# Kernel optimization log

Hardware: AMD Instinct MI355X
Metric: run time of the kernel (lower is better)

Reference implementation:

```python
import jax, jax.numpy as jnp
import numpy as np

N_NODES = 100000
N_EDGES = 640000
D_IN = 128
D_OUT = 128


def setup_inputs() -> dict:
    key = jax.random.key(0)
    k1, k2, k3, k4, k5 = jax.random.split(key, 5)
    feats = jax.random.normal(k1, (N_NODES, D_IN), dtype=jnp.float32)
    src = jax.random.randint(k2, (N_EDGES,), 0, N_NODES, dtype=jnp.int32)
    dst = jax.random.randint(k3, (N_EDGES,), 0, N_NODES, dtype=jnp.int32)
    # Xavier-normal-ish init (gain for relu = sqrt(2))
    std = float(np.sqrt(2.0) * np.sqrt(2.0 / (D_IN + D_OUT)))
    linear_skip_weight = jax.random.normal(k4, (D_OUT, D_IN), dtype=jnp.float32) * std
    linear_msg_weight = jax.random.normal(k5, (D_OUT, D_IN), dtype=jnp.float32) * std
    linear_skip_bias = jnp.zeros((D_OUT,), dtype=jnp.float32)
    linear_msg_bias = jnp.zeros((D_OUT,), dtype=jnp.float32)
    return {
        "feats": feats,
        "src": src,
        "dst": dst,
        "linear_skip_weight": linear_skip_weight,
        "linear_skip_bias": linear_skip_bias,
        "linear_msg_weight": linear_msg_weight,
        "linear_msg_bias": linear_msg_bias,
    }


def reference(feats, src, dst, linear_skip_weight, linear_skip_bias,
              linear_msg_weight, linear_msg_bias):
    n = feats.shape[0]
    # degree from scatter-add of edge weights (ones) at source rows
    deg = jax.ops.segment_sum(jnp.ones_like(src, dtype=feats.dtype), src,
                              num_segments=n)
    deg_inv_sqrt = jnp.where(deg > 0, jax.lax.rsqrt(jnp.maximum(deg, 1.0)) * (deg > 0), 0.0)
    deg_inv_sqrt = jnp.where(deg > 0, deg ** -0.5, 0.0)
    # normalize source features, gather along edges, scatter-sum to dst
    feat_src = feats * deg_inv_sqrt[:, None]           # [N, D_IN]
    msgs = feat_src[src]                               # [E, D_IN]
    rst = jax.ops.segment_sum(msgs, dst, num_segments=n)  # [N, D_IN]
    rst = rst * deg_inv_sqrt[:, None]
    rst_ = rst @ linear_msg_weight.T + linear_msg_bias
    skip_x = feats @ linear_skip_weight.T + linear_skip_bias
    return rst_ + skip_x
```

## Files before the change

### kernel.cpp

```cpp
#include <hip/hip_runtime.h>

#define N_NODES 100000
#define N_EDGES 640000
#define D 128
#define NB ((N_NODES + 1023) / 1024)
#define BKT_C 16
#define OVF_CAP 32768

typedef short v8s __attribute__((ext_vector_type(8)));
typedef float v4f __attribute__((ext_vector_type(4)));

__device__ __forceinline__ unsigned short f2bf(float x) {
    unsigned int u = __builtin_bit_cast(unsigned int, x);
    u += 0x7fffu + ((u >> 16) & 1u);
    return (unsigned short)(u >> 16);
}
__device__ __forceinline__ float bf2f(unsigned int hi) {
    return __builtin_bit_cast(float, hi << 16);
}

__global__ __launch_bounds__(256) void k_zero(int4* __restrict__ pk4,
                                              int* __restrict__ ovf_cnt) {
    int i = blockIdx.x * blockDim.x + threadIdx.x;
    if (i < N_NODES / 4) pk4[i] = make_int4(0, 0, 0, 0);
    if (i == 0) *ovf_cnt = 0;
}

__global__ __launch_bounds__(256) void k_pre(const float* __restrict__ feats,
                                             const float* __restrict__ Wm,
                                             const float* __restrict__ Ws,
                                             const float* __restrict__ bmsg,
                                             const float* __restrict__ bskip,
                                             const int* __restrict__ src,
                                             const int* __restrict__ dst,
                                             unsigned int* __restrict__ pk,
                                             unsigned short* __restrict__ Bcat,
                                             float* __restrict__ bias,
                                             char* __restrict__ fsbase,
                                             int fs_stride,
                                             int* __restrict__ bucket,
                                             int* __restrict__ ovf_cnt,
                                             int2* __restrict__ ovf) {
    int i = blockIdx.x * blockDim.x + threadIdx.x;
    if (i < D * D) {
        int j = i >> 7;
        int k = i & 127;
        Bcat[j * 256 + k]       = f2bf(Wm[i]);
        Bcat[j * 256 + 128 + k] = f2bf(Ws[i]);
    }
    if (i < D) bias[i] = bmsg[i] + bskip[i];
    if (i < N_EDGES) {
        int s = src[i];
        int d = dst[i];
        atomicAdd(&pk[s], 1u);
        unsigned int old = atomicAdd(&pk[d], 0x10000u);
        if (bucket) {
            unsigned int p = old >> 16;
            if (p < BKT_C) {
                bucket[d * BKT_C + (int)p] = s;
            } else {
                int q = atomicAdd(ovf_cnt, 1);
                if (q < OVF_CAP) ovf[q] = make_int2(d, s);
            }
        }
    }
    int g = i * 8;
    int row = g >> 7;
    int col = g & 127;
    if (row < N_NODES) {
        const float4* sp = (const float4*)(feats + g);
        float4 x = sp[0], y = sp[1];
        uint4 p;
        p.x = (unsigned)f2bf(x.x) | ((unsigned)f2bf(x.y) << 16);
        p.y = (unsigned)f2bf(x.z) | ((unsigned)f2bf(x.w) << 16);
        p.z = (unsigned)f2bf(y.x) | ((unsigned)f2bf(y.y) << 16);
        p.w = (unsigned)f2bf(y.z) | ((unsigned)f2bf(y.w) << 16);
        *(uint4*)(fsbase + (size_t)row * fs_stride + col * 2) = p;
    }
}

__global__ __launch_bounds__(256) void k_fused2(const char* __restrict__ featsh,
                                                const unsigned int* __restrict__ pk,
                                                const int* __restrict__ bucket,
                                                const int* __restrict__ ovf_cnt,
                                                const int2* __restrict__ ovf,
                                                const unsigned short* __restrict__ Bcat,
                                                const float* __restrict__ bias,
                                                float* __restrict__ outf) {
    __shared__ unsigned short aggh[128][132];
    int tid = threadIdx.x;
    int lane = tid & 63;
    int w = tid >> 6;
    int n0 = blockIdx.x * 128;
    int grp = lane >> 4;
    int sub = lane & 15;

#pragma unroll 2
    for (int j = 0; j < 32; ++j) {
        int wid = n0 + w * 32 + j;
        int widc = wid < N_NODES ? wid : N_NODES - 1;
        unsigned int pkn = pk[widc];
        int cnt = (int)(pkn >> 16);
        int m = cnt < BKT_C ? cnt : BKT_C;
        const int* bk = bucket + widc * BKT_C;

        int4 bq = *(const int4*)(bk + grp * 4);
        int e0 = grp * 4;
        bool a0 = e0 < m, a1 = e0 + 1 < m, a2 = e0 + 2 < m, a3 = e0 + 3 < m;
        int sA = a0 ? bq.x : 0; float gA = a0 ? 1.0f : 0.0f;
        int sB = a1 ? bq.y : 0; float gB = a1 ? 1.0f : 0.0f;
        int sC = a2 ? bq.z : 0; float gC = a2 ? 1.0f : 0.0f;
        int sD = a3 ? bq.w : 0; float gD = a3 ? 1.0f : 0.0f;

        unsigned int pA = pk[sA];
        unsigned int pB = pk[sB];
        unsigned int pC = pk[sC];
        unsigned int pD = pk[sD];
        uint4 vA = *(const uint4*)(featsh + (size_t)sA * 256 + sub * 16);
        uint4 vB = *(const uint4*)(featsh + (size_t)sB * 256 + sub * 16);
        uint4 vC = *(const uint4*)(featsh + (size_t)sC * 256 + sub * 16);
        uint4 vD = *(const uint4*)(featsh + (size_t)sD * 256 + sub * 16);

        float scA = gA * rsqrtf(fmaxf((float)(pA & 0xffffu), 1.0f));
        float scB = gB * rsqrtf(fmaxf((float)(pB & 0xffffu), 1.0f));
        float scC = gC * rsqrtf(fmaxf((float)(pC & 0xffffu), 1.0f));
        float scD = gD * rsqrtf(fmaxf((float)(pD & 0xffffu), 1.0f));

        float acc[8];
#pragma unroll
        for (int i = 0; i < 8; i++) acc[i] = 0.f;
        acc[0] += bf2f(vA.x & 0xffffu) * scA; acc[1] += bf2f(vA.x >> 16) * scA;
        acc[2] += bf2f(vA.y & 0xffffu) * scA; acc[3] += bf2f(vA.y >> 16) * scA;
        acc[4] += bf2f(vA.z & 0xffffu) * scA; acc[5] += bf2f(vA.z >> 16) * scA;
        acc[6] += bf2f(vA.w & 0xffffu) * scA; acc[7] += bf2f(vA.w >> 16) * scA;
        acc[0] += bf2f(vB.x & 0xffffu) * scB; acc[1] += bf2f(vB.x >> 16) * scB;
        acc[2] += bf2f(vB.y & 0xffffu) * scB; acc[3] += bf2f(vB.y >> 16) * scB;
        acc[4] += bf2f(vB.z & 0xffffu) * scB; acc[5] += bf2f(vB.z >> 16) * scB;
        acc[6] += bf2f(vB.w & 0xffffu) * scB; acc[7] += bf2f(vB.w >> 16) * scB;
        acc[0] += bf2f(vC.x & 0xffffu) * scC; acc[1] += bf2f(vC.x >> 16) * scC;
        acc[2] += bf2f(vC.y & 0xffffu) * scC; acc[3] += bf2f(vC.y >> 16) * scC;
        acc[4] += bf2f(vC.z & 0xffffu) * scC; acc[5] += bf2f(vC.z >> 16) * scC;
        acc[6] += bf2f(vC.w & 0xffffu) * scC; acc[7] += bf2f(vC.w >> 16) * scC;
        acc[0] += bf2f(vD.x & 0xffffu) * scD; acc[1] += bf2f(vD.x >> 16) * scD;
        acc[2] += bf2f(vD.y & 0xffffu) * scD; acc[3] += bf2f(vD.y >> 16) * scD;
        acc[4] += bf2f(vD.z & 0xffffu) * scD; acc[5] += bf2f(vD.z >> 16) * scD;
        acc[6] += bf2f(vD.w & 0xffffu) * scD; acc[7] += bf2f(vD.w >> 16) * scD;

        if (cnt > BKT_C) {
            int no = *ovf_cnt;
            if (no > OVF_CAP) no = OVF_CAP;
            for (int i = grp; i < no; i += 4) {
                int2 p = ovf[i];
                if (p.x == widc) {
                    float sc = rsqrtf((float)(pk[p.y] & 0xffffu));
                    uint4 v = *(const uint4*)(featsh + (size_t)p.y * 256 + sub * 16);
                    acc[0] += bf2f(v.x & 0xffffu) * sc; acc[1] += bf2f(v.x >> 16) * sc;
                    acc[2] += bf2f(v.y & 0xffffu) * sc; acc[3] += bf2f(v.y >> 16) * sc;
                    acc[4] += bf2f(v.z & 0xffffu) * sc; acc[5] += bf2f(v.z >> 16) * sc;
                    acc[6] += bf2f(v.w & 0xffffu) * sc; acc[7] += bf2f(v.w >> 16) * sc;
                }
            }
        }

#pragma unroll
        for (int i = 0; i < 8; i++) {
            acc[i] += __shfl_xor(acc[i], 16);
            acc[i] += __shfl_xor(acc[i], 32);
        }
        if (grp == 0) {
            int dsrc = (int)(pkn & 0xffffu);
            float scn = (dsrc > 0) ? rsqrtf((float)dsrc) : 0.0f;
            uint4 p;
            p.x = (unsigned)f2bf(acc[0] * scn) | ((unsigned)f2bf(acc[1] * scn) << 16);
            p.y = (unsigned)f2bf(acc[2] * scn) | ((unsigned)f2bf(acc[3] * scn) << 16);
            p.z = (unsigned)f2bf(acc[4] * scn) | ((unsigned)f2bf(acc[5] * scn) << 16);
            p.w = (unsigned)f2bf(acc[6] * scn) | ((unsigned)f2bf(acc[7] * scn) << 16);
            *(uint4*)(&aggh[w * 32 + j][sub * 8]) = p;
        }
    }

    int q = grp;
    int lr = sub;
    int r0 = n0 + w * 32 + lr;      int r0c = r0 < N_NODES ? r0 : N_NODES - 1;
    int r1 = r0 + 16;               int r1c = r1 < N_NODES ? r1 : N_NODES - 1;
    const char* a0p = featsh + (size_t)r0c * 256 + q * 16;
    const char* a1p = featsh + (size_t)r1c * 256 + q * 16;

    v4f acc2[2][8];
#pragma unroll
    for (int mt = 0; mt < 2; mt++)
#pragma unroll
        for (int t = 0; t < 8; t++) acc2[mt][t] = (v4f){0.f, 0.f, 0.f, 0.f};

#pragma unroll
    for (int kk = 0; kk < 8; kk++) {
        v8s a0, a1;
        if (kk < 4) {
            a0 = *(const v8s*)(&aggh[w * 32 + lr][q * 8 + kk * 32]);
            a1 = *(const v8s*)(&aggh[w * 32 + 16 + lr][q * 8 + kk * 32]);
        } else {
            a0 = *(const v8s*)(a0p + (kk - 4) * 64);
            a1 = *(const v8s*)(a1p + (kk - 4) * 64);
        }
#pragma unroll
        for (int t = 0; t < 8; t++) {
            v8s b = *(const v8s*)(Bcat + (t * 16 + lr) * 256 + kk * 32 + q * 8);
            acc2[0][t] = __builtin_amdgcn_mfma_f32_16x16x32_bf16(a0, b, acc2[0][t], 0, 0, 0);
            acc2[1][t] = __builtin_amdgcn_mfma_f32_16x16x32_bf16(a1, b, acc2[1][t], 0, 0, 0);
        }
    }

#pragma unroll
    for (int t = 0; t < 8; t++) {
        float bv = bias[t * 16 + lr];
#pragma unroll
        for (int mt = 0; mt < 2; mt++) {
            int rowb = n0 + w * 32 + mt * 16 + q * 4;
#pragma unroll
            for (int r = 0; r < 4; r++) {
                int row = rowb + r;
                if (row < N_NODES)
                    outf[(size_t)row * 128 + t * 16 + lr] = acc2[mt][t][r] + bv;
            }
        }
    }
}

__device__ __forceinline__ void agg_edge(const char* outb,
                                         const unsigned int* pk,
                                         int s, int sub, float* acc) {
    float sc = rsqrtf((float)(pk[s] & 0xffffu));
    uint4 v = *(const uint4*)(outb + (size_t)s * 512 + 256 + sub * 16);
    acc[0] += bf2f(v.x & 0xffffu) * sc;
    acc[1] += bf2f(v.x >> 16) * sc;
    acc[2] += bf2f(v.y & 0xffffu) * sc;
    acc[3] += bf2f(v.y >> 16) * sc;
    acc[4] += bf2f(v.z & 0xffffu) * sc;
    acc[5] += bf2f(v.z >> 16) * sc;
    acc[6] += bf2f(v.w & 0xffffu) * sc;
    acc[7] += bf2f(v.w >> 16) * sc;
}

__device__ __forceinline__ void agg_acc(uint4 v, float sc, float* acc) {
    acc[0] += bf2f(v.x & 0xffffu) * sc;
    acc[1] += bf2f(v.x >> 16) * sc;
    acc[2] += bf2f(v.y & 0xffffu) * sc;
    acc[3] += bf2f(v.y >> 16) * sc;
    acc[4] += bf2f(v.z & 0xffffu) * sc;
    acc[5] += bf2f(v.z >> 16) * sc;
    acc[6] += bf2f(v.w & 0xffffu) * sc;
    acc[7] += bf2f(v.w >> 16) * sc;
}

__device__ __forceinline__ void agg_finish(char* outb, int wid,
                                           unsigned int pkn, int grp, int sub,
                                           float* acc) {
#pragma unroll
    for (int i = 0; i < 8; i++) {
        acc[i] += __shfl_xor(acc[i], 16);
        acc[i] += __shfl_xor(acc[i], 32);
    }
    if (grp == 0) {
        int dsrc = (int)(pkn & 0xffffu);
        float scn = (dsrc > 0) ? rsqrtf((float)dsrc) : 0.0f;
        uint4 p;
        p.x = (unsigned)f2bf(acc[0] * scn) | ((unsigned)f2bf(acc[1] * scn) << 16);
        p.y = (unsigned)f2bf(acc[2] * scn) | ((unsigned)f2bf(acc[3] * scn) << 16);
        p.z = (unsigned)f2bf(acc[4] * scn) | ((unsigned)f2bf(acc[5] * scn) << 16);
        p.w = (unsigned)f2bf(acc[6] * scn) | ((unsigned)f2bf(acc[7] * scn) << 16);
        *(uint4*)(outb + (size_t)wid * 512 + sub * 16) = p;
    }
}

__global__ __launch_bounds__(256) void k_agg_bkt(char* __restrict__ outb,
                                                 const unsigned int* __restrict__ pk,
                                                 const int* __restrict__ bucket,
                                                 const int* __restrict__ ovf_cnt,
                                                 const int2* __restrict__ ovf) {
    int wid = (int)((blockIdx.x * (unsigned)blockDim.x + threadIdx.x) >> 6);
    int lane = threadIdx.x & 63;
    if (wid >= N_NODES) return;
    int grp = lane >> 4;
    int sub = lane & 15;
    unsigned int pkn = pk[wid];
    int cnt = (int)(pkn >> 16);
    int m = cnt < BKT_C ? cnt : BKT_C;
    const int* bk = bucket + wid * BKT_C;

    int4 bq = *(const int4*)(bk + grp * 4);
    int e0 = grp * 4;

    bool a0 = e0 < m, a1 = e0 + 1 < m, a2 = e0 + 2 < m, a3 = e0 + 3 < m;
    int sA = a0 ? bq.x : 0; float gA = a0 ? 1.0f : 0.0f;
    int sB = a1 ? bq.y : 0; float gB = a1 ? 1.0f : 0.0f;
    int sC = a2 ? bq.z : 0; float gC = a2 ? 1.0f : 0.0f;
    int sD = a3 ? bq.w : 0; float gD = a3 ? 1.0f : 0.0f;

    unsigned int pA = pk[sA];
    unsigned int pB = pk[sB];
    unsigned int pC = pk[sC];
    unsigned int pD = pk[sD];
    uint4 vA = *(const uint4*)(outb + (size_t)sA * 512 + 256 + sub * 16);
    uint4 vB = *(const uint4*)(outb + (size_t)sB * 512 + 256 + sub * 16);
    uint4 vC = *(const uint4*)(outb + (size_t)sC * 512 + 256 + sub * 16);
    uint4 vD = *(const uint4*)(outb + (size_t)sD * 512 + 256 + sub * 16);

    float scA = gA * rsqrtf(fmaxf((float)(pA & 0xffffu), 1.0f));
    float scB = gB * rsqrtf(fmaxf((float)(pB & 0xffffu), 1.0f));
    float scC = gC * rsqrtf(fmaxf((float)(pC & 0xffffu), 1.0f));
    float scD = gD * rsqrtf(fmaxf((float)(pD & 0xffffu), 1.0f));

    float acc[8];
#pragma unroll
    for (int i = 0; i < 8; i++) acc[i] = 0.f;
    agg_acc(vA, scA, acc);
    agg_acc(vB, scB, acc);
    agg_acc(vC, scC, acc);
    agg_acc(vD, scD, acc);

    if (cnt > BKT_C) {
        int no = *ovf_cnt;
        if (no > OVF_CAP) no = OVF_CAP;
        for (int i = grp; i < no; i += 4) {
            int2 p = ovf[i];
            if (p.x == wid) agg_edge(outb, pk, p.y, sub, acc);
        }
    }
    agg_finish(outb, wid, pkn, grp, sub, acc);
}

__global__ __launch_bounds__(256) void k_scan1(const unsigned int* __restrict__ pk,
                                               int* __restrict__ rowptr,
                                               int* __restrict__ bsums) {
    __shared__ int sd[256];
    int t = threadIdx.x;
    int i0 = blockIdx.x * 1024 + t * 4;
    int v[4];
    int s = 0;
#pragma unroll
    for (int q = 0; q < 4; q++) {
        int i = i0 + q;
        v[q] = (i < N_NODES) ? (int)(pk[i] >> 16) : 0;
        s += v[q];
    }
    sd[t] = s;
    __syncthreads();
    for (int off = 1; off < 256; off <<= 1) {
        int y = (t >= off) ? sd[t - off] : 0;
        __syncthreads();
        sd[t] += y;
        __syncthreads();
    }
    int run = sd[t] - s;
    if (t == 255) bsums[blockIdx.x] = sd[255];
#pragma unroll
    for (int q = 0; q < 4; q++) {
        int i = i0 + q;
        if (i < N_NODES) rowptr[i] = run;
        run += v[q];
    }
}

__global__ __launch_bounds__(128) void k_scan2(int* __restrict__ bsums) {
    __shared__ int sd[128];
    int t = threadIdx.x;
    int v = (t < NB) ? bsums[t] : 0;
    sd[t] = v;
    __syncthreads();
    for (int off = 1; off < 128; off <<= 1) {
        int y = (t >= off) ? sd[t - off] : 0;
        __syncthreads();
        sd[t] += y;
        __syncthreads();
    }
    if (t < NB) bsums[t] = sd[t] - v;
}

__global__ __launch_bounds__(256) void k_scan3(const int* __restrict__ bsums,
                                               int* __restrict__ rowptr) {
    int add = bsums[blockIdx.x];
    int i0 = blockIdx.x * 1024 + threadIdx.x * 4;
#pragma unroll
    for (int q = 0; q < 4; q++) {
        int i = i0 + q;
        if (i < N_NODES) rowptr[i] += add;
    }
}

__global__ __launch_bounds__(256) void k_fill(const int* __restrict__ src,
                                              const int* __restrict__ dst,
                                              int* __restrict__ rowptr,
                                              int* __restrict__ csr_src) {
    int e = blockIdx.x * blockDim.x + threadIdx.x;
    if (e < N_EDGES) {
        int p = atomicAdd(&rowptr[dst[e]], 1);
        csr_src[p] = src[e];
    }
}

__global__ __launch_bounds__(256) void k_agg_csr(char* __restrict__ outb,
                                                 const unsigned int* __restrict__ pk,
                                                 const int* __restrict__ rowptr,
                                                 const int* __restrict__ csr_src) {
    int wid = (int)((blockIdx.x * (unsigned)blockDim.x + threadIdx.x) >> 6);
    int lane = threadIdx.x & 63;
    if (wid >= N_NODES) return;
    int grp = lane >> 4;
    int sub = lane & 15;
    int start = (wid == 0) ? 0 : rowptr[wid - 1];
    int end = rowptr[wid];
    float acc[8];
#pragma unroll
    for (int i = 0; i < 8; i++) acc[i] = 0.f;
    for (int base = start; base < end; base += 4) {
        int e = base + grp;
        if (e < end) agg_edge(outb, pk, csr_src[e], sub, acc);
    }
    agg_finish(outb, wid, pk[wid], grp, sub, acc);
}

__global__ __launch_bounds__(256) void k_gemm(const unsigned short* __restrict__ Bcat,
                                              const float* __restrict__ bias,
                                              float* __restrict__ outf) {
    __shared__ unsigned short Bl[128][264];
    const char* Ab = (const char*)outf;
    int tid = threadIdx.x;
    int lane = tid & 63;
    int w = tid >> 6;
    int n0 = blockIdx.x * 128;

    for (int i = tid; i < 128 * 32; i += 256) {
        int r = i >> 5, c = i & 31;
        *(uint4*)(&Bl[r][c * 8]) = *(const uint4*)(Bcat + r * 256 + c * 8);
    }
    __syncthreads();

    int q = lane >> 4;
    int lr = lane & 15;

    int r0 = n0 + w * 32 + lr;      if (r0 > N_NODES - 1) r0 = N_NODES - 1;
    int r1 = n0 + w * 32 + 16 + lr; if (r1 > N_NODES - 1) r1 = N_NODES - 1;
    const char* a0p = Ab + (size_t)r0 * 512 + q * 16;
    const char* a1p = Ab + (size_t)r1 * 512 + q * 16;

    v4f acc[2][8];
#pragma unroll
    for (int mt = 0; mt < 2; mt++)
#pragma unroll
        for (int t = 0; t < 8; t++) acc[mt][t] = (v4f){0.f, 0.f, 0.f, 0.f};

#pragma unroll
    for (int kk = 0; kk < 8; kk++) {
        v8s a0 = *(const v8s*)(a0p + kk * 64);
        v8s a1 = *(const v8s*)(a1p + kk * 64);
#pragma unroll
        for (int t = 0; t < 8; t++) {
            v8s b = *(const v8s*)(&Bl[t * 16 + lr][kk * 32 + q * 8]);
            acc[0][t] = __builtin_amdgcn_mfma_f32_16x16x32_bf16(a0, b, acc[0][t], 0, 0, 0);
            acc[1][t] = __builtin_amdgcn_mfma_f32_16x16x32_bf16(a1, b, acc[1][t], 0, 0, 0);
        }
    }

#pragma unroll
    for (int t = 0; t < 8; t++) {
        float bv = bias[t * 16 + lr];
#pragma unroll
        for (int mt = 0; mt < 2; mt++) {
            int rowb = n0 + w * 32 + mt * 16 + q * 4;
#pragma unroll
            for (int r = 0; r < 4; r++) {
                int row = rowb + r;
                if (row < N_NODES)
                    outf[(size_t)row * 128 + t * 16 + lr] = acc[mt][t][r] + bv;
            }
        }
    }
}

extern "C" void kernel_launch(void* const* d_in, const int* in_sizes, int n_in,
                              void* d_out, int out_size, void* d_ws, size_t ws_size,
                              hipStream_t stream) {
    const float* feats = (const float*)d_in[0];
    const int*   src   = (const int*)d_in[1];
    const int*   dst   = (const int*)d_in[2];
    const float* Wskip = (const float*)d_in[3];
    const float* bskip = (const float*)d_in[4];
    const float* Wmsg  = (const float*)d_in[5];
    const float* bmsg  = (const float*)d_in[6];

    char* w = (char*)d_ws;

    bool pathC = ws_size >= (size_t)32728320;
    bool pathA = ws_size >= (size_t)7128320;

    if (pathC) {
        unsigned int*   pk      = (unsigned int*)w;
        int*            ovf_cnt = (int*)(w + 400000);
        unsigned short* Bcat    = (unsigned short*)(w + 400128);
        float*          bias    = (float*)(w + 465664);
        int*            bucket  = (int*)(w + 466176);
        int2*           ovf     = (int2*)(w + 6866176);
        char*           featsh  = w + 7128320;

        hipLaunchKernelGGL(k_zero, dim3((N_NODES / 4 + 255) / 256), dim3(256), 0,
                           stream, (int4*)pk, ovf_cnt);
        hipLaunchKernelGGL(k_pre, dim3((N_NODES * (D / 8) + 255) / 256), dim3(256),
                           0, stream, feats, Wmsg, Wskip, bmsg, bskip, src, dst, pk,
                           Bcat, bias, featsh, 256, bucket, ovf_cnt, ovf);
        hipLaunchKernelGGL(k_fused2, dim3((N_NODES + 127) / 128), dim3(256), 0,
                           stream, featsh, pk, bucket, ovf_cnt, ovf, Bcat, bias,
                           (float*)d_out);
    } else if (pathA) {
        unsigned int*   pk      = (unsigned int*)w;
        int*            ovf_cnt = (int*)(w + 400000);
        unsigned short* Bcat    = (unsigned short*)(w + 400128);
        float*          bias    = (float*)(w + 465664);
        int*            bucket  = (int*)(w + 466176);
        int2*           ovf     = (int2*)(w + 6866176);

        hipLaunchKernelGGL(k_zero, dim3((N_NODES / 4 + 255) / 256), dim3(256), 0,
                           stream, (int4*)pk, ovf_cnt);
        hipLaunchKernelGGL(k_pre, dim3((N_NODES * (D / 8) + 255) / 256), dim3(256),
                           0, stream, feats, Wmsg, Wskip, bmsg, bskip, src, dst, pk,
                           Bcat, bias, (char*)d_out + 256, 512, bucket, ovf_cnt, ovf);
        hipLaunchKernelGGL(k_agg_bkt, dim3((N_NODES * 64 + 255) / 256), dim3(256), 0,
                           stream, (char*)d_out, pk, bucket, ovf_cnt, ovf);
        hipLaunchKernelGGL(k_gemm, dim3((N_NODES + 127) / 128), dim3(256), 0, stream,
                           Bcat, bias, (float*)d_out);
    } else {
        unsigned int*   pk      = (unsigned int*)w;
        int*            rowptr  = (int*)(w + 400000);
        int*            bsums   = (int*)(w + 800128);
        unsigned short* Bcat    = (unsigned short*)(w + 800640);
        float*          bias    = (float*)(w + 866176);
        int*            csr_src = (int*)(w + 866688);

        hipLaunchKernelGGL(k_zero, dim3((N_NODES / 4 + 255) / 256), dim3(256), 0,
                           stream, (int4*)pk, (int*)(w + 400000) );
        hipLaunchKernelGGL(k_pre, dim3((N_NODES * (D / 8) + 255) / 256), dim3(256),
                           0, stream, feats, Wmsg, Wskip, bmsg, bskip, src, dst, pk,
                           Bcat, bias, (char*)d_out + 256, 512, (int*)nullptr,
                           (int*)nullptr, (int2*)nullptr);
        hipLaunchKernelGGL(k_scan1, dim3(NB), dim3(256), 0, stream, pk, rowptr,
                           bsums);
        hipLaunchKernelGGL(k_scan2, dim3(1), dim3(128), 0, stream, bsums);
        hipLaunchKernelGGL(k_scan3, dim3(NB), dim3(256), 0, stream, bsums, rowptr);
        hipLaunchKernelGGL(k_fill, dim3((N_EDGES + 255) / 256), dim3(256), 0, stream,
                           src, dst, rowptr, csr_src);
        hipLaunchKernelGGL(k_agg_csr, dim3((N_NODES * 64 + 255) / 256), dim3(256), 0,
                           stream, (char*)d_out, pk, rowptr, csr_src);
        hipLaunchKernelGGL(k_gemm, dim3((N_NODES + 127) / 128), dim3(256), 0, stream,
                           Bcat, bias, (float*)d_out);
    }
}
```

Baseline: 270.0 us.

## Split fused aggregate+GEMM into wave-per-node aggregation and LDS-staged GEMM

Replaces the single fused kernel, where each block aggregated 128 nodes serially into LDS and then ran MFMA, with two kernels. The first uses one wave per node with full-grid parallelism and writes bf16 aggregates into the output buffer. The second loads them back, with the weight matrix staged in LDS, to run the MFMA GEMM. The bucket array is now zeroed so that unused slots can be loaded without masking the indices. This gains parallelism and latency hiding for the gather, at the cost of an extra kernel launch, an intermediate global round trip and a larger zeroing pass.

Measured after the change: 234.7 us, median of 2. 1.15x faster.

```diff
diff --git a/kernel.cpp b/kernel.cpp
--- a/kernel.cpp
+++ b/kernel.cpp
@@ -20,10 +20,12 @@
 }
 
 __global__ __launch_bounds__(256) void k_zero(int4* __restrict__ pk4,
+                                              int4* __restrict__ bkt4,
                                               int* __restrict__ ovf_cnt) {
     int i = blockIdx.x * blockDim.x + threadIdx.x;
     if (i < N_NODES / 4) pk4[i] = make_int4(0, 0, 0, 0);
-    if (i == 0) *ovf_cnt = 0;
+    if (bkt4 && i < N_NODES * BKT_C / 4) bkt4[i] = make_int4(0, 0, 0, 0);
+    if (i == 0 && ovf_cnt) *ovf_cnt = 0;
 }
 
 __global__ __launch_bounds__(256) void k_pre(const float* __restrict__ feats,
@@ -79,134 +81,145 @@
     }
 }
 
-__global__ __launch_bounds__(256) void k_fused2(const char* __restrict__ featsh,
-                                                const unsigned int* __restrict__ pk,
-                                                const int* __restrict__ bucket,
-                                                const int* __restrict__ ovf_cnt,
-                                                const int2* __restrict__ ovf,
+__global__ __launch_bounds__(256) void k_agg_c(char* __restrict__ outb,
+                                               const char* __restrict__ featsh,
+                                               const unsigned int* __restrict__ pk,
+                                               const int* __restrict__ bucket,
+                                               const int* __restrict__ ovf_cnt,
+                                               const int2* __restrict__ ovf) {
+    int wid = (int)((blockIdx.x * (unsigned)blockDim.x + threadIdx.x) >> 6);
+    int lane = threadIdx.x & 63;
+    if (wid >= N_NODES) return;
+    int grp = lane >> 4;
+    int sub = lane & 15;
+
+    int4 bq = *(const int4*)(bucket + wid * BKT_C + grp * 4);
+    unsigned int pkn = pk[wid];
+
+    int sA = bq.x, sB = bq.y, sC = bq.z, sD = bq.w;
+    unsigned int pA = pk[sA];
+    unsigned int pB = pk[sB];
+    unsigned int pC = pk[sC];
+    unsigned int pD = pk[sD];
+    uint4 vA = *(const uint4*)(featsh + (size_t)sA * 256 + sub * 16);
+    uint4 vB = *(const uint4*)(featsh + (size_t)sB * 256 + sub * 16);
+    uint4 vC = *(const uint4*)(featsh + (size_t)sC * 256 + sub * 16);
+    uint4 vD = *(const uint4*)(featsh + (size_t)sD * 256 + sub * 16);
+
+    int cnt = (int)(pkn >> 16);
+    int m = cnt < BKT_C ? cnt : BKT_C;
+    int e0 = grp * 4;
+    float gA = (e0 < m) ? 1.0f : 0.0f;
+    float gB = (e0 + 1 < m) ? 1.0f : 0.0f;
+    float gC = (e0 + 2 < m) ? 1.0f : 0.0f;
+    float gD = (e0 + 3 < m) ? 1.0f : 0.0f;
+
+    float scA = gA * rsqrtf(fmaxf((float)(pA & 0xffffu), 1.0f));
+    float scB = gB * rsqrtf(fmaxf((float)(pB & 0xffffu), 1.0f));
+    float scC = gC * rsqrtf(fmaxf((float)(pC & 0xffffu), 1.0f));
+    float scD = gD * rsqrtf(fmaxf((float)(pD & 0xffffu), 1.0f));
+
+    float acc[8];
+#pragma unroll
+    for (int i = 0; i < 8; i++) acc[i] = 0.f;
+    acc[0] += bf2f(vA.x & 0xffffu) * scA; acc[1] += bf2f(vA.x >> 16) * scA;
+    acc[2] += bf2f(vA.y & 0xffffu) * scA; acc[3] += bf2f(vA.y >> 16) * scA;
+    acc[4] += bf2f(vA.z & 0xffffu) * scA; acc[5] += bf2f(vA.z >> 16) * scA;
+    acc[6] += bf2f(vA.w & 0xffffu) * scA; acc[7] += bf2f(vA.w >> 16) * scA;
+    acc[0] += bf2f(vB.x & 0xffffu) * scB; acc[1] += bf2f(vB.x >> 16) * scB;
+    acc[2] += bf2f(vB.y & 0xffffu) * scB; acc[3] += bf2f(vB.y >> 16) * scB;
+    acc[4] += bf2f(vB.z & 0xffffu) * scB; acc[5] += bf2f(vB.z >> 16) * scB;
+    acc[6] += bf2f(vB.w & 0xffffu) * scB; acc[7] += bf2f(vB.w >> 16) * scB;
+    acc[0] += bf2f(vC.x & 0xffffu) * scC; acc[1] += bf2f(vC.x >> 16) * scC;
+    acc[2] += bf2f(vC.y & 0xffffu) * scC; acc[3] += bf2f(vC.y >> 16) * scC;
+    acc[4] += bf2f(vC.z & 0xffffu) * scC; acc[5] += bf2f(vC.z >> 16) * scC;
+    acc[6] += bf2f(vC.w & 0xffffu) * scC; acc[7] += bf2f(vC.w >> 16) * scC;
+    acc[0] += bf2f(vD.x & 0xffffu) * scD; acc[1] += bf2f(vD.x >> 16) * scD;
+    acc[2] += bf2f(vD.y & 0xffffu) * scD; acc[3] += bf2f(vD.y >> 16) * scD;
+    acc[4] += bf2f(vD.z & 0xffffu) * scD; acc[5] += bf2f(vD.z >> 16) * scD;
+    acc[6] += bf2f(vD.w & 0xffffu) * scD; acc[7] += bf2f(vD.w >> 16) * scD;
+
+    if (cnt > BKT_C) {
+        int no = *ovf_cnt;
+        if (no > OVF_CAP) no = OVF_CAP;
+        for (int i = grp; i < no; i += 4) {
+            int2 p = ovf[i];
+            if (p.x == wid) {
+                float sc = rsqrtf((float)(pk[p.y] & 0xffffu));
+                uint4 v = *(const uint4*)(featsh + (size_t)p.y * 256 + sub * 16);
+                acc[0] += bf2f(v.x & 0xffffu) * sc; acc[1] += bf2f(v.x >> 16) * sc;
+                acc[2] += bf2f(v.y & 0xffffu) * sc; acc[3] += bf2f(v.y >> 16) * sc;
+                acc[4] += bf2f(v.z & 0xffffu) * sc; acc[5] += bf2f(v.z >> 16) * sc;
+                acc[6] += bf2f(v.w & 0xffffu) * sc; acc[7] += bf2f(v.w >> 16) * sc;
+            }
+        }
+    }
+
+#pragma unroll
+    for (int i = 0; i < 8; i++) {
+        acc[i] += __shfl_xor(acc[i], 16);
+        acc[i] += __shfl_xor(acc[i], 32);
+    }
+    if (grp == 0) {
+        int dsrc = (int)(pkn & 0xffffu);
+        float scn = (dsrc > 0) ? rsqrtf((float)dsrc) : 0.0f;
+        uint4 p;
+        p.x = (unsigned)f2bf(acc[0] * scn) | ((unsigned)f2bf(acc[1] * scn) << 16);
+        p.y = (unsigned)f2bf(acc[2] * scn) | ((unsigned)f2bf(acc[3] * scn) << 16);
+        p.z = (unsigned)f2bf(acc[4] * scn) | ((unsigned)f2bf(acc[5] * scn) << 16);
+        p.w = (unsigned)f2bf(acc[6] * scn) | ((unsigned)f2bf(acc[7] * scn) << 16);
+        *(uint4*)(outb + (size_t)wid * 512 + sub * 16) = p;
+    }
+}
+
+__global__ __launch_bounds__(256) void k_gemm_c(const char* __restrict__ featsh,
                                                 const unsigned short* __restrict__ Bcat,
                                                 const float* __restrict__ bias,
                                                 float* __restrict__ outf) {
-    __shared__ unsigned short aggh[128][132];
+    __shared__ unsigned short Bl[128][264];
+    const char* Ab = (const char*)outf;
     int tid = threadIdx.x;
     int lane = tid & 63;
     int w = tid >> 6;
     int n0 = blockIdx.x * 128;
-    int grp = lane >> 4;
-    int sub = lane & 15;
-
-#pragma unroll 2
-    for (int j = 0; j < 32; ++j) {
-        int wid = n0 + w * 32 + j;
-        int widc = wid < N_NODES ? wid : N_NODES - 1;
-        unsigned int pkn = pk[widc];
-        int cnt = (int)(pkn >> 16);
-        int m = cnt < BKT_C ? cnt : BKT_C;
-        const int* bk = bucket + widc * BKT_C;
-
-        int4 bq = *(const int4*)(bk + grp * 4);
-        int e0 = grp * 4;
-        bool a0 = e0 < m, a1 = e0 + 1 < m, a2 = e0 + 2 < m, a3 = e0 + 3 < m;
-        int sA = a0 ? bq.x : 0; float gA = a0 ? 1.0f : 0.0f;
-        int sB = a1 ? bq.y : 0; float gB = a1 ? 1.0f : 0.0f;
-        int sC = a2 ? bq.z : 0; float gC = a2 ? 1.0f : 0.0f;
-        int sD = a3 ? bq.w : 0; float gD = a3 ? 1.0f : 0.0f;
-
-        unsigned int pA = pk[sA];
-        unsigned int pB = pk[sB];
-        unsigned int pC = pk[sC];
-        unsigned int pD = pk[sD];
-        uint4 vA = *(const uint4*)(featsh + (size_t)sA * 256 + sub * 16);
-        uint4 vB = *(const uint4*)(featsh + (size_t)sB * 256 + sub * 16);
-        uint4 vC = *(const uint4*)(featsh + (size_t)sC * 256 + sub * 16);
-        uint4 vD = *(const uint4*)(featsh + (size_t)sD * 256 + sub * 16);
-
-        float scA = gA * rsqrtf(fmaxf((float)(pA & 0xffffu), 1.0f));
-        float scB = gB * rsqrtf(fmaxf((float)(pB & 0xffffu), 1.0f));
-        float scC = gC * rsqrtf(fmaxf((float)(pC & 0xffffu), 1.0f));
-        float scD = gD * rsqrtf(fmaxf((float)(pD & 0xffffu), 1.0f));
-
-        float acc[8];
-#pragma unroll
-        for (int i = 0; i < 8; i++) acc[i] = 0.f;
-        acc[0] += bf2f(vA.x & 0xffffu) * scA; acc[1] += bf2f(vA.x >> 16) * scA;
-        acc[2] += bf2f(vA.y & 0xffffu) * scA; acc[3] += bf2f(vA.y >> 16) * scA;
-        acc[4] += bf2f(vA.z & 0xffffu) * scA; acc[5] += bf2f(vA.z >> 16) * scA;
-        acc[6] += bf2f(vA.w & 0xffffu) * scA; acc[7] += bf2f(vA.w >> 16) * scA;
-        acc[0] += bf2f(vB.x & 0xffffu) * scB; acc[1] += bf2f(vB.x >> 16) * scB;
-        acc[2] += bf2f(vB.y & 0xffffu) * scB; acc[3] += bf2f(vB.y >> 16) * scB;
-        acc[4] += bf2f(vB.z & 0xffffu) * scB; acc[5] += bf2f(vB.z >> 16) * scB;
-        acc[6] += bf2f(vB.w & 0xffffu) * scB; acc[7] += bf2f(vB.w >> 16) * scB;
-        acc[0] += bf2f(vC.x & 0xffffu) * scC; acc[1] += bf2f(vC.x >> 16) * scC;
-        acc[2] += bf2f(vC.y & 0xffffu) * scC; acc[3] += bf2f(vC.y >> 16) * scC;
-        acc[4] += bf2f(vC.z & 0xffffu) * scC; acc[5] += bf2f(vC.z >> 16) * scC;
-        acc[6] += bf2f(vC.w & 0xffffu) * scC; acc[7] += bf2f(vC.w >> 16) * scC;
-        acc[0] += bf2f(vD.x & 0xffffu) * scD; acc[1] += bf2f(vD.x >> 16) * scD;
-        acc[2] += bf2f(vD.y & 0xffffu) * scD; acc[3] += bf2f(vD.y >> 16) * scD;
-        acc[4] += bf2f(vD.z & 0xffffu) * scD; acc[5] += bf2f(vD.z >> 16) * scD;
-        acc[6] += bf2f(vD.w & 0xffffu) * scD; acc[7] += bf2f(vD.w >> 16) * scD;
-
-        if (cnt > BKT_C) {
-            int no = *ovf_cnt;
-            if (no > OVF_CAP) no = OVF_CAP;
-            for (int i = grp; i < no; i += 4) {
-                int2 p = ovf[i];
-                if (p.x == widc) {
-                    float sc = rsqrtf((float)(pk[p.y] & 0xffffu));
-                    uint4 v = *(const uint4*)(featsh + (size_t)p.y * 256 + sub * 16);
-                    acc[0] += bf2f(v.x & 0xffffu) * sc; acc[1] += bf2f(v.x >> 16) * sc;
-                    acc[2] += bf2f(v.y & 0xffffu) * sc; acc[3] += bf2f(v.y >> 16) * sc;
-                    acc[4] += bf2f(v.z & 0xffffu) * sc; acc[5] += bf2f(v.z >> 16) * sc;
-                    acc[6] += bf2f(v.w & 0xffffu) * sc; acc[7] += bf2f(v.w >> 16) * sc;
-                }
-            }
-        }
-
-#pragma unroll
-        for (int i = 0; i < 8; i++) {
-            acc[i] += __shfl_xor(acc[i], 16);
-            acc[i] += __shfl_xor(acc[i], 32);
-        }
-        if (grp == 0) {
-            int dsrc = (int)(pkn & 0xffffu);
-            float scn = (dsrc > 0) ? rsqrtf((float)dsrc) : 0.0f;
-            uint4 p;
-            p.x = (unsigned)f2bf(acc[0] * scn) | ((unsigned)f2bf(acc[1] * scn) << 16);
-            p.y = (unsigned)f2bf(acc[2] * scn) | ((unsigned)f2bf(acc[3] * scn) << 16);
-            p.z = (unsigned)f2bf(acc[4] * scn) | ((unsigned)f2bf(acc[5] * scn) << 16);
-            p.w = (unsigned)f2bf(acc[6] * scn) | ((unsigned)f2bf(acc[7] * scn) << 16);
-            *(uint4*)(&aggh[w * 32 + j][sub * 8]) = p;
-        }
-    }
-
-    int q = grp;
-    int lr = sub;
-    int r0 = n0 + w * 32 + lr;      int r0c = r0 < N_NODES ? r0 : N_NODES - 1;
-    int r1 = r0 + 16;               int r1c = r1 < N_NODES ? r1 : N_NODES - 1;
-    const char* a0p = featsh + (size_t)r0c * 256 + q * 16;
-    const char* a1p = featsh + (size_t)r1c * 256 + q * 16;
-
-    v4f acc2[2][8];
+
+    for (int i = tid; i < 128 * 32; i += 256) {
+        int r = i >> 5, c = i & 31;
+        *(uint4*)(&Bl[r][c * 8]) = *(const uint4*)(Bcat + r * 256 + c * 8);
+    }
+    __syncthreads();
+
+    int q = lane >> 4;
+    int lr = lane & 15;
+
+    int r0 = n0 + w * 32 + lr;      if (r0 > N_NODES - 1) r0 = N_NODES - 1;
+    int r1 = n0 + w * 32 + 16 + lr; if (r1 > N_NODES - 1) r1 = N_NODES - 1;
+    const char* g0p = Ab + (size_t)r0 * 512 + q * 16;
+    const char* g1p = Ab + (size_t)r1 * 512 + q * 16;
+    const char* f0p = featsh + (size_t)r0 * 256 + q * 16;
+    const char* f1p = featsh + (size_t)r1 * 256 + q * 16;
+
+    v4f acc[2][8];
 #pragma unroll
     for (int mt = 0; mt < 2; mt++)
 #pragma unroll
-        for (int t = 0; t < 8; t++) acc2[mt][t] = (v4f){0.f, 0.f, 0.f, 0.f};
+        for (int t = 0; t < 8; t++) acc[mt][t] = (v4f){0.f, 0.f, 0.f, 0.f};
 
 #pragma unroll
     for (int kk = 0; kk < 8; kk++) {
         v8s a0, a1;
         if (kk < 4) {
-            a0 = *(const v8s*)(&aggh[w * 32 + lr][q * 8 + kk * 32]);
-            a1 = *(const v8s*)(&aggh[w * 32 + 16 + lr][q * 8 + kk * 32]);
+            a0 = *(const v8s*)(g0p + kk * 64);
+            a1 = *(const v8s*)(g1p + kk * 64);
         } else {
-            a0 = *(const v8s*)(a0p + (kk - 4) * 64);
-            a1 = *(const v8s*)(a1p + (kk - 4) * 64);
+            a0 = *(const v8s*)(f0p + (kk - 4) * 64);
+            a1 = *(const v8s*)(f1p + (kk - 4) * 64);
         }
 #pragma unroll
         for (int t = 0; t < 8; t++) {
-            v8s b = *(const v8s*)(Bcat + (t * 16 + lr) * 256 + kk * 32 + q * 8);
-            acc2[0][t] = __builtin_amdgcn_mfma_f32_16x16x32_bf16(a0, b, acc2[0][t], 0, 0, 0);
-            acc2[1][t] = __builtin_amdgcn_mfma_f32_16x16x32_bf16(a1, b, acc2[1][t], 0, 0, 0);
+            v8s b = *(const v8s*)(&Bl[t * 16 + lr][kk * 32 + q * 8]);
+            acc[0][t] = __builtin_amdgcn_mfma_f32_16x16x32_bf16(a0, b, acc[0][t], 0, 0, 0);
+            acc[1][t] = __builtin_amdgcn_mfma_f32_16x16x32_bf16(a1, b, acc[1][t], 0, 0, 0);
         }
     }
 
@@ -220,7 +233,7 @@
             for (int r = 0; r < 4; r++) {
                 int row = rowb + r;
                 if (row < N_NODES)
-                    outf[(size_t)row * 128 + t * 16 + lr] = acc2[mt][t][r] + bv;
+                    outf[(size_t)row * 128 + t * 16 + lr] = acc[mt][t][r] + bv;
             }
         }
     }
@@ -502,14 +515,15 @@
         int2*           ovf     = (int2*)(w + 6866176);
         char*           featsh  = w + 7128320;
 
-        hipLaunchKernelGGL(k_zero, dim3((N_NODES / 4 + 255) / 256), dim3(256), 0,
-                           stream, (int4*)pk, ovf_cnt);
+        hipLaunchKernelGGL(k_zero, dim3((N_NODES * BKT_C / 4 + 255) / 256),
+                           dim3(256), 0, stream, (int4*)pk, (int4*)bucket, ovf_cnt);
         hipLaunchKernelGGL(k_pre, dim3((N_NODES * (D / 8) + 255) / 256), dim3(256),
                            0, stream, feats, Wmsg, Wskip, bmsg, bskip, src, dst, pk,
                            Bcat, bias, featsh, 256, bucket, ovf_cnt, ovf);
-        hipLaunchKernelGGL(k_fused2, dim3((N_NODES + 127) / 128), dim3(256), 0,
-                           stream, featsh, pk, bucket, ovf_cnt, ovf, Bcat, bias,
-                           (float*)d_out);
+        hipLaunchKernelGGL(k_agg_c, dim3((N_NODES * 64 + 255) / 256), dim3(256), 0,
+                           stream, (char*)d_out, featsh, pk, bucket, ovf_cnt, ovf);
+        hipLaunchKernelGGL(k_gemm_c, dim3((N_NODES + 127) / 128), dim3(256), 0,
+                           stream, featsh, Bcat, bias, (float*)d_out);
     } else if (pathA) {
         unsigned int*   pk      = (unsigned int*)w;
         int*            ovf_cnt = (int*)(w + 400000);
@@ -519,7 +533,7 @@
         int2*           ovf     = (int2*)(w + 6866176);
 
         hipLaunchKernelGGL(k_zero, dim3((N_NODES / 4 + 255) / 256), dim3(256), 0,
-                           stream, (int4*)pk, ovf_cnt);
+                           stream, (int4*)pk, (int4*)nullptr, ovf_cnt);
         hipLaunchKernelGGL(k_pre, dim3((N_NODES * (D / 8) + 255) / 256), dim3(256),
                            0, stream, feats, Wmsg, Wskip, bmsg, bskip, src, dst, pk,
                            Bcat, bias, (char*)d_out + 256, 512, bucket, ovf_cnt, ovf);
@@ -536,7 +550,7 @@
         int*            csr_src = (int*)(w + 866688);
 
         hipLaunchKernelGGL(k_zero, dim3((N_NODES / 4 + 255) / 256), dim3(256), 0,
-                           stream, (int4*)pk, (int*)(w + 400000) );
+                           stream, (int4*)pk, (int4*)nullptr, (int*)nullptr);
         hipLaunchKernelGGL(k_pre, dim3((N_NODES * (D / 8) + 255) / 256), dim3(256),
                            0, stream, feats, Wmsg, Wskip, bmsg, bskip, src, dst, pk,
                            Bcat, bias, (char*)d_out + 256, 512, (int*)nullptr,
```
